# Kernel tuning notes

Hardware: AMD Instinct MI355X
Metric: run time of the kernel (lower is better)

## Reference

```python
import jax, jax.numpy as jnp
import numpy as np

EMBED = 1024
HEADS = 16
HEAD_DIM = EMBED // HEADS


def setup_inputs() -> dict:
    key = jax.random.key(0)
    ks = jax.random.split(key, 6)
    s = 1.0 / np.sqrt(EMBED)
    return {
        "x": jax.random.normal(ks[0], (4, 4096, EMBED), dtype=jnp.float32),
        "Wq": jax.random.normal(ks[1], (EMBED, EMBED), dtype=jnp.float32) * s,
        "Wk": jax.random.normal(ks[2], (EMBED, EMBED), dtype=jnp.float32) * s,
        "Wv": jax.random.normal(ks[3], (EMBED, EMBED), dtype=jnp.float32) * s,
        "Wo": jax.random.normal(ks[4], (EMBED, EMBED), dtype=jnp.float32) * s,
        "bo": jax.random.normal(ks[5], (EMBED,), dtype=jnp.float32) * 0.01,
    }


def reference(x, Wq, Wk, Wv, Wo, bo):
    # Faithful to the torch module, including its cross-head attention:
    # the einsum subscripts in the original treat the HEAD axis as the
    # attended (q/k) axis and the SEQUENCE axis as a batch axis.
    N, L, E = x.shape
    H, D = HEADS, HEAD_DIM
    q = (x @ Wq).reshape(N, L, H, D)
    k = (x @ Wk).reshape(N, L, H, D)
    v = (x @ Wv).reshape(N, L, H, D)
    # energy[n, l, hq, hk] = sum_d q[n, l, hq, d] * k[n, l, hk, d]
    energy = jnp.einsum('nlqd,nlkd->nlqk', q, k)  # (N, L, H, H)
    scale = jnp.asarray(E, x.dtype) ** 0.5
    attn = jax.nn.softmax(energy / scale, axis=-1)
    out = jnp.einsum('nlqk,nlkd->nlqd', attn, v).reshape(N, L, E)
    return out @ Wo + bo
```

## Files before the change

kernel.cpp:

```cpp
#include <hip/hip_runtime.h>


typedef unsigned short u16;
typedef unsigned int u32;

typedef __bf16 bf16x8 __attribute__((ext_vector_type(8)));
typedef float f32x4 __attribute__((ext_vector_type(4)));

__device__ __forceinline__ u16 f2bf(float f) {
  u32 u = __float_as_uint(f);
  u += 0x7fffu + ((u >> 16) & 1u);
  return (u16)(u >> 16);
}
__device__ __forceinline__ float bflo(u32 u) { return __uint_as_float(u << 16); }
__device__ __forceinline__ float bfhi(u32 u) { return __uint_as_float(u & 0xffff0000u); }

__device__ __forceinline__ void load_lds16(const u16* g, u16* l) {
  __builtin_amdgcn_global_load_lds(
      (const __attribute__((address_space(1))) u32*)g,
      (__attribute__((address_space(3))) u32*)l, 16, 0, 0);
}

__global__ __launch_bounds__(256) void prep_kernel(
    const float* __restrict__ x, u16* __restrict__ xb,
    const float* __restrict__ Wq, const float* __restrict__ Wk,
    const float* __restrict__ Wv, const float* __restrict__ Wo,
    u16* __restrict__ Wt, u16* __restrict__ Wot) {
  const int bid = blockIdx.x, tid = threadIdx.x;
  if (bid < 8192) {
    size_t i = (size_t)bid * 256 + tid;
    const float4* p = (const float4*)x;
    float4 a = p[2 * i], b = p[2 * i + 1];
    u32 w0 = (u32)f2bf(a.x) | ((u32)f2bf(a.y) << 16);
    u32 w1 = (u32)f2bf(a.z) | ((u32)f2bf(a.w) << 16);
    u32 w2 = (u32)f2bf(b.x) | ((u32)f2bf(b.y) << 16);
    u32 w3 = (u32)f2bf(b.z) | ((u32)f2bf(b.w) << 16);
    *(uint4*)(xb + 8 * i) = make_uint4(w0, w1, w2, w3);
  } else {
    __shared__ float tile[32][33];
    const int b = bid - 8192;
    const int z = b >> 10, rem = b & 1023;
    const float* W = (z == 0) ? Wq : (z == 1) ? Wk : (z == 2) ? Wv : Wo;
    u16* D = (z < 3) ? (Wt + (size_t)z * 1024 * 1024) : Wot;
    const int n0 = (rem & 31) * 32, k0 = (rem >> 5) * 32;
    const int tx = tid & 31, ty = tid >> 5;
#pragma unroll
    for (int i = 0; i < 4; i++)
      tile[ty + i * 8][tx] = W[(size_t)(k0 + ty + i * 8) * 1024 + n0 + tx];
    __syncthreads();
#pragma unroll
    for (int i = 0; i < 4; i++)
      D[(size_t)(n0 + ty + i * 8) * 1024 + k0 + tx] = f2bf(tile[tx][ty + i * 8]);
  }
}

template <int WRITE_MODE>
__global__ __launch_bounds__(256) void gemm_bt(const u16* __restrict__ A,
                                               const u16* __restrict__ Bt,
                                               void* __restrict__ Cv,
                                               const float* __restrict__ bias,
                                               int N, int K) {
  constexpr int BM = 128, BN = 128, BK = 64;
  __shared__ u16 As[BM * BK];
  __shared__ u16 Bs[BN * BK];
  const int t = threadIdx.x;
  const int lane = t & 63;
  const int wave = t >> 6;
  const int wr = wave >> 1, wc = wave & 1;
  const int bid = blockIdx.x;
  const int bm = (((bid & 7) << 4) + ((bid >> 3) & 15)) * BM;
  const int bn = (bid >> 7) * BN;
  const int lrow = lane & 15, lq = lane >> 4;
  const int lx = lrow & 7;

  f32x4 acc[4][4];
#pragma unroll
  for (int i = 0; i < 4; i++)
#pragma unroll
    for (int j = 0; j < 4; j++) acc[i][j] = 0.0f;

  const u16* Ap = A + (size_t)bm * K;
  const u16* Bp = Bt + (size_t)bn * K;

  int srow[4], scol[4];
#pragma unroll
  for (int i = 0; i < 4; i++) {
    int s = t + 256 * i;
    srow[i] = s >> 3;
    scol[i] = ((s & 7) ^ (srow[i] & 7)) << 3;
  }

  for (int k0 = 0; k0 < K; k0 += BK) {
#pragma unroll
    for (int i = 0; i < 4; i++)
      load_lds16(Ap + (size_t)srow[i] * K + k0 + scol[i], &As[(t + 256 * i) * 8]);
#pragma unroll
    for (int i = 0; i < 4; i++)
      load_lds16(Bp + (size_t)srow[i] * K + k0 + scol[i], &Bs[(t + 256 * i) * 8]);
    __syncthreads();
#pragma unroll
    for (int ks = 0; ks < BK; ks += 32) {
      const int kq = (ks >> 3) + lq;
      const int kqs = (kq ^ lx) << 3;
      bf16x8 af[4], bg[4];
#pragma unroll
      for (int i = 0; i < 4; i++)
        af[i] = *(const bf16x8*)&As[(wr * 64 + i * 16 + lrow) * BK + kqs];
#pragma unroll
      for (int j = 0; j < 4; j++)
        bg[j] = *(const bf16x8*)&Bs[(wc * 64 + j * 16 + lrow) * BK + kqs];
#pragma unroll
      for (int i = 0; i < 4; i++)
#pragma unroll
        for (int j = 0; j < 4; j++)
          acc[i][j] = __builtin_amdgcn_mfma_f32_16x16x32_bf16(af[i], bg[j], acc[i][j], 0, 0, 0);
    }
    __syncthreads();
  }

#pragma unroll
  for (int i = 0; i < 4; i++) {
#pragma unroll
    for (int j = 0; j < 4; j++) {
      int col = bn + wc * 64 + j * 16 + lrow;
#pragma unroll
      for (int r = 0; r < 4; r++) {
        int row = bm + wr * 64 + i * 16 + lq * 4 + r;
        if (WRITE_MODE == 0) {
          ((u16*)Cv)[(size_t)row * N + col] = f2bf(acc[i][j][r]);
        } else {
          ((float*)Cv)[(size_t)row * N + col] = acc[i][j][r] + bias[col];
        }
      }
    }
  }
}

__device__ __forceinline__ void load16f(const u16* p, float* f) {
  const uint4* u = (const uint4*)p;
  uint4 a = u[0], b = u[1];
  f[0] = bflo(a.x);  f[1] = bfhi(a.x);  f[2] = bflo(a.y);  f[3] = bfhi(a.y);
  f[4] = bflo(a.z);  f[5] = bfhi(a.z);  f[6] = bflo(a.w);  f[7] = bfhi(a.w);
  f[8] = bflo(b.x);  f[9] = bfhi(b.x);  f[10] = bflo(b.y); f[11] = bfhi(b.y);
  f[12] = bflo(b.z); f[13] = bfhi(b.z); f[14] = bflo(b.w); f[15] = bfhi(b.w);
}

__global__ __launch_bounds__(256) void attn_kernel(const u16* __restrict__ QKV,
                                                   u16* __restrict__ AO) {
  __shared__ u16 kv[4][2048];
  const int t = threadIdx.x, lane = t & 63, wave = t >> 6;
  const int sub = lane & 3;
  const int tok = blockIdx.x * 4 + wave;

  const u16* base = QKV + (size_t)tok * 3072;
  uint4 k0 = ((const uint4*)(base + 1024))[2 * lane];
  uint4 k1 = ((const uint4*)(base + 1024))[2 * lane + 1];
  uint4 v0 = ((const uint4*)(base + 2048))[2 * lane];
  uint4 v1 = ((const uint4*)(base + 2048))[2 * lane + 1];
  float qf[16];
  load16f(base + lane * 16, qf);
  ((uint4*)&kv[wave][0])[2 * lane] = k0;
  ((uint4*)&kv[wave][0])[2 * lane + 1] = k1;
  ((uint4*)&kv[wave][1024])[2 * lane] = v0;
  ((uint4*)&kv[wave][1024])[2 * lane + 1] = v1;

  float e[16];
#pragma unroll
  for (int hk = 0; hk < 16; hk++) {
    float kf[16];
    load16f(&kv[wave][hk * 64 + sub * 16], kf);
    float s = 0.f;
#pragma unroll
    for (int i = 0; i < 16; i++) s = fmaf(qf[i], kf[i], s);
    s += __shfl_xor(s, 1);
    s += __shfl_xor(s, 2);
    e[hk] = s;
  }

  float m = e[0];
#pragma unroll
  for (int hk = 1; hk < 16; hk++) m = fmaxf(m, e[hk]);
  float sum = 0.f;
#pragma unroll
  for (int hk = 0; hk < 16; hk++) {
    float p = __expf((e[hk] - m) * 0.03125f);
    e[hk] = p;
    sum += p;
  }
  float inv = 1.0f / sum;

  float o[16];
#pragma unroll
  for (int i = 0; i < 16; i++) o[i] = 0.f;
#pragma unroll
  for (int hk = 0; hk < 16; hk++) {
    float a = e[hk] * inv;
    float vf[16];
    load16f(&kv[wave][1024 + hk * 64 + sub * 16], vf);
#pragma unroll
    for (int i = 0; i < 16; i++) o[i] = fmaf(a, vf[i], o[i]);
  }

  u32 w[8];
#pragma unroll
  for (int i = 0; i < 8; i++)
    w[i] = (u32)f2bf(o[2 * i]) | ((u32)f2bf(o[2 * i + 1]) << 16);
  uint4* dst = (uint4*)(AO + (size_t)tok * 1024 + lane * 16);
  dst[0] = make_uint4(w[0], w[1], w[2], w[3]);
  dst[1] = make_uint4(w[4], w[5], w[6], w[7]);
}


extern "C" void kernel_launch(void* const* d_in, const int* in_sizes, int n_in,
                              void* d_out, int out_size, void* d_ws, size_t ws_size,
                              hipStream_t stream) {
  const float* x = (const float*)d_in[0];
  const float* Wq = (const float*)d_in[1];
  const float* Wk = (const float*)d_in[2];
  const float* Wv = (const float*)d_in[3];
  const float* Wo = (const float*)d_in[4];
  const float* bo = (const float*)d_in[5];
  float* out = (float*)d_out;

  char* ws = (char*)d_ws;
  u16* Xb  = (u16*)(ws);
  u16* Wt  = (u16*)(ws + 33554432);
  u16* Wot = (u16*)(ws + 39845888);
  u16* QKV = (u16*)(ws + 41943040);
  u16* AO  = (u16*)(ws + 142606336);

  prep_kernel<<<12288, 256, 0, stream>>>(x, Xb, Wq, Wk, Wv, Wo, Wt, Wot);
  gemm_bt<0><<<3072, 256, 0, stream>>>(Xb, Wt, QKV, nullptr, 3072, 1024);
  attn_kernel<<<4096, 256, 0, stream>>>(QKV, AO);
  gemm_bt<1><<<1024, 256, 0, stream>>>(AO, Wot, out, bo, 1024, 1024);
}
```

Before: 328.8 us.

## Replace GEMMs with 256x256 eight-wave kernel using double-buffered LDS pipeline

Both GEMMs move from a 128x128, 4-wave tile with a single LDS buffer to a 256x256, 8-wave tile with 128KB of dynamic LDS. Each K-tile is split into A and B halves that are prefetched two tiles ahead with async global-to-LDS loads, interleaved with four MFMA quadrant phases under raised wave priority. The aim is to raise arithmetic intensity per global load and hide load latency behind matrix math. In exchange it uses far more LDS, allows fewer resident blocks per CU, and relies on hand-placed barriers and vmcnt waits whose correctness is delicate.

```diff
diff --git a/kernel.cpp b/kernel.cpp
--- a/kernel.cpp
+++ b/kernel.cpp
@@ -54,86 +54,155 @@
   }
 }
 
+
+#define SYNC_IN()                                      \
+  __builtin_amdgcn_s_barrier();                        \
+  asm volatile("s_waitcnt lgkmcnt(0)" ::: "memory");   \
+  __builtin_amdgcn_sched_barrier(0)
+
+#define MM(FM, FN, Af, Bf)                                                      \
+  do {                                                                          \
+    __builtin_amdgcn_s_setprio(1);                                              \
+    _Pragma("unroll") for (int m_ = 0; m_ < 4; m_++)                            \
+    _Pragma("unroll") for (int j_ = 0; j_ < 2; j_++)                            \
+    _Pragma("unroll") for (int k_ = 0; k_ < 2; k_++)                            \
+        acc[(FM) + m_][(FN) + j_] = __builtin_amdgcn_mfma_f32_16x16x32_bf16(    \
+            Af[m_][k_], Bf[j_][k_], acc[(FM) + m_][(FN) + j_], 0, 0, 0);        \
+    __builtin_amdgcn_s_setprio(0);                                              \
+  } while (0)
+
 template <int WRITE_MODE>
-__global__ __launch_bounds__(256) void gemm_bt(const u16* __restrict__ A,
-                                               const u16* __restrict__ Bt,
-                                               void* __restrict__ Cv,
-                                               const float* __restrict__ bias,
-                                               int N, int K) {
-  constexpr int BM = 128, BN = 128, BK = 64;
-  __shared__ u16 As[BM * BK];
-  __shared__ u16 Bs[BN * BK];
+__global__ __launch_bounds__(512, 2) void gemm8(const u16* __restrict__ A,
+                                                const u16* __restrict__ Bt,
+                                                void* __restrict__ Cv,
+                                                const float* __restrict__ bias,
+                                                int N, int K) {
+  extern __shared__ __align__(16) u16 smem[];
   const int t = threadIdx.x;
   const int lane = t & 63;
   const int wave = t >> 6;
-  const int wr = wave >> 1, wc = wave & 1;
+  const int wm = wave >> 2;
+  const int wn = wave & 3;
+  const int lrow = lane & 15, lq = lane >> 4;
+  const int wm64 = wm * 64, wn32 = wn * 32;
+
   const int bid = blockIdx.x;
-  const int bm = (((bid & 7) << 4) + ((bid >> 3) & 15)) * BM;
-  const int bn = (bid >> 7) * BN;
-  const int lrow = lane & 15, lq = lane >> 4;
-  const int lx = lrow & 7;
-
-  f32x4 acc[4][4];
-#pragma unroll
-  for (int i = 0; i < 4; i++)
+  const int bm_t = ((bid & 7) << 3) | ((bid >> 3) & 7);
+  const int bn_t = bid >> 6;
+  const size_t bm = (size_t)bm_t * 256;
+  const size_t bn = (size_t)bn_t * 256;
+
+  const u16* Ap = A + bm * K;
+  const u16* Bp = Bt + bn * K;
+  const size_t halfK = (size_t)128 * K;
+  const int NT = K >> 6;
+
+  int srow[2], soff[2], sdst[2];
+#pragma unroll
+  for (int i = 0; i < 2; i++) {
+    const int s = (i << 9) + t;
+    srow[i] = s >> 3;
+    soff[i] = ((s & 7) ^ (srow[i] & 7)) << 3;
+    sdst[i] = s << 3;
+  }
+
+#define RG(buf, op, h) (smem + ((((buf) << 2) | ((op) << 1) | (h)) << 13))
+
+  auto STG = [&](const u16* Gp, int kt, u16* L) {
+#pragma unroll
+    for (int i = 0; i < 2; i++)
+      load_lds16(Gp + (size_t)srow[i] * K + (kt << 6) + soff[i], L + sdst[i]);
+  };
+  auto LDA = [&](bf16x8 (&f)[4][2], const u16* base) {
+#pragma unroll
+    for (int m = 0; m < 4; m++) {
+      const int rh = wm64 + m * 16 + lrow;
+      const int ro = rh << 6, rx = rh & 7;
+#pragma unroll
+      for (int ks = 0; ks < 2; ks++)
+        f[m][ks] = *(const bf16x8*)&base[ro + ((((ks << 2) + lq) ^ rx) << 3)];
+    }
+  };
+  auto LDB = [&](bf16x8 (&f)[2][2], const u16* base) {
+#pragma unroll
+    for (int j = 0; j < 2; j++) {
+      const int ch = wn32 + j * 16 + lrow;
+      const int co = ch << 6, cx = ch & 7;
+#pragma unroll
+      for (int ks = 0; ks < 2; ks++)
+        f[j][ks] = *(const bf16x8*)&base[co + ((((ks << 2) + lq) ^ cx) << 3)];
+    }
+  };
+
+  f32x4 acc[8][4];
+#pragma unroll
+  for (int i = 0; i < 8; i++)
 #pragma unroll
     for (int j = 0; j < 4; j++) acc[i][j] = 0.0f;
 
-  const u16* Ap = A + (size_t)bm * K;
-  const u16* Bp = Bt + (size_t)bn * K;
-
-  int srow[4], scol[4];
-#pragma unroll
-  for (int i = 0; i < 4; i++) {
-    int s = t + 256 * i;
-    srow[i] = s >> 3;
-    scol[i] = ((s & 7) ^ (srow[i] & 7)) << 3;
-  }
-
-  for (int k0 = 0; k0 < K; k0 += BK) {
-#pragma unroll
-    for (int i = 0; i < 4; i++)
-      load_lds16(Ap + (size_t)srow[i] * K + k0 + scol[i], &As[(t + 256 * i) * 8]);
-#pragma unroll
-    for (int i = 0; i < 4; i++)
-      load_lds16(Bp + (size_t)srow[i] * K + k0 + scol[i], &Bs[(t + 256 * i) * 8]);
-    __syncthreads();
-#pragma unroll
-    for (int ks = 0; ks < BK; ks += 32) {
-      const int kq = (ks >> 3) + lq;
-      const int kqs = (kq ^ lx) << 3;
-      bf16x8 af[4], bg[4];
-#pragma unroll
-      for (int i = 0; i < 4; i++)
-        af[i] = *(const bf16x8*)&As[(wr * 64 + i * 16 + lrow) * BK + kqs];
-#pragma unroll
-      for (int j = 0; j < 4; j++)
-        bg[j] = *(const bf16x8*)&Bs[(wc * 64 + j * 16 + lrow) * BK + kqs];
-#pragma unroll
-      for (int i = 0; i < 4; i++)
-#pragma unroll
-        for (int j = 0; j < 4; j++)
-          acc[i][j] = __builtin_amdgcn_mfma_f32_16x16x32_bf16(af[i], bg[j], acc[i][j], 0, 0, 0);
-    }
-    __syncthreads();
-  }
-
-#pragma unroll
-  for (int i = 0; i < 4; i++) {
-#pragma unroll
-    for (int j = 0; j < 4; j++) {
-      int col = bn + wc * 64 + j * 16 + lrow;
+  bf16x8 af[4][2], bf0[2][2], bf1[2][2];
+
+  STG(Ap, 0, RG(0, 0, 0));
+  STG(Bp, 0, RG(0, 1, 0));
+  STG(Bp + halfK, 0, RG(0, 1, 1));
+  STG(Ap + halfK, 0, RG(0, 0, 1));
+  STG(Ap, 1, RG(1, 0, 0));
+  STG(Bp, 1, RG(1, 1, 0));
+  STG(Bp + halfK, 1, RG(1, 1, 1));
+  asm volatile("s_waitcnt vmcnt(0)" ::: "memory");
+  __builtin_amdgcn_s_barrier();
+
+  for (int tt = 0; tt < NT; ++tt) {
+    const int p = tt & 1;
+    int t1 = tt + 1; if (t1 >= NT) t1 -= NT;
+    int t2 = tt + 2; if (t2 >= NT) t2 -= NT;
+    const int q1 = p ^ 1, q2 = p;
+
+    LDA(af, RG(p, 0, 0));
+    LDB(bf0, RG(p, 1, 0));
+    STG(Ap + halfK, t1, RG(q1, 0, 1));
+    SYNC_IN();
+    MM(0, 0, af, bf0);
+    __builtin_amdgcn_s_barrier();
+
+    LDB(bf1, RG(p, 1, 1));
+    STG(Ap, t2, RG(q2, 0, 0));
+    SYNC_IN();
+    MM(0, 2, af, bf1);
+    __builtin_amdgcn_s_barrier();
+
+    LDA(af, RG(p, 0, 1));
+    STG(Bp, t2, RG(q2, 1, 0));
+    SYNC_IN();
+    MM(4, 2, af, bf1);
+    __builtin_amdgcn_s_barrier();
+
+    STG(Bp + halfK, t2, RG(q2, 1, 1));
+    SYNC_IN();
+    MM(4, 0, af, bf0);
+    asm volatile("s_waitcnt vmcnt(6)" ::: "memory");
+    __builtin_amdgcn_s_barrier();
+  }
+  asm volatile("s_waitcnt vmcnt(0)" ::: "memory");
+
+#pragma unroll
+  for (int fm = 0; fm < 8; fm++) {
+    const int MH = fm >> 2, fmr = fm & 3;
+#pragma unroll
+    for (int fn = 0; fn < 4; fn++) {
+      const int NH = fn >> 1, fnr = fn & 1;
+      const size_t col = bn + NH * 128 + wn32 + fnr * 16 + lrow;
 #pragma unroll
       for (int r = 0; r < 4; r++) {
-        int row = bm + wr * 64 + i * 16 + lq * 4 + r;
-        if (WRITE_MODE == 0) {
-          ((u16*)Cv)[(size_t)row * N + col] = f2bf(acc[i][j][r]);
-        } else {
-          ((float*)Cv)[(size_t)row * N + col] = acc[i][j][r] + bias[col];
-        }
+        const size_t row = bm + MH * 128 + wm64 + fmr * 16 + lq * 4 + r;
+        if (WRITE_MODE == 0)
+          ((u16*)Cv)[row * N + col] = f2bf(acc[fm][fn][r]);
+        else
+          ((float*)Cv)[row * N + col] = acc[fm][fn][r] + bias[col];
       }
     }
   }
+#undef RG
 }
 
 __device__ __forceinline__ void load16f(const u16* p, float* f) {
@@ -229,8 +298,13 @@
   u16* QKV = (u16*)(ws + 41943040);
   u16* AO  = (u16*)(ws + 142606336);
 
+  hipFuncSetAttribute(reinterpret_cast<const void*>(&gemm8<0>),
+                      hipFuncAttributeMaxDynamicSharedMemorySize, 131072);
+  hipFuncSetAttribute(reinterpret_cast<const void*>(&gemm8<1>),
+                      hipFuncAttributeMaxDynamicSharedMemorySize, 131072);
+
   prep_kernel<<<12288, 256, 0, stream>>>(x, Xb, Wq, Wk, Wv, Wo, Wt, Wot);
-  gemm_bt<0><<<3072, 256, 0, stream>>>(Xb, Wt, QKV, nullptr, 3072, 1024);
+  gemm8<0><<<768, 512, 131072, stream>>>(Xb, Wt, QKV, nullptr, 3072, 1024);
   attn_kernel<<<4096, 256, 0, stream>>>(QKV, AO);
-  gemm_bt<1><<<1024, 256, 0, stream>>>(AO, Wot, out, bo, 1024, 1024);
-}
+  gemm8<1><<<256, 512, 131072, stream>>>(AO, Wot, out, bo, 1024, 1024);
+}
```

Measured after the change: 299.5 us. 1.1x faster.
